# Kernel tuning notes

Measured on AMD Instinct MI355X. Metric: run time of the kernel, lower is better.

Reference implementation:

```python
import jax, jax.numpy as jnp
import numpy as np

B, L, E, H = 2, 2048, 2048, 16
HD = E // H  # 128
ROPE_BASE = 10000.0


def setup_inputs() -> dict:
    key = jax.random.key(0)
    k1, k2, k3 = jax.random.split(key, 3)
    x = jax.random.normal(k1, (B, L, E), dtype=jnp.float32)
    position_ids = jnp.tile(jnp.arange(L, dtype=jnp.int32)[None, :], (B, 1))
    # Linear weights stored as [in, out] so y = x @ W + b (equals torch x @ W.T + b)
    W_attn = jax.random.normal(k2, (E, 3 * E), dtype=jnp.float32) * (1.0 / np.sqrt(E))
    b_attn = jnp.zeros((3 * E,), dtype=jnp.float32)
    W_proj = jax.random.normal(k3, (E, E), dtype=jnp.float32) * (1.0 / np.sqrt(E))
    b_proj = jnp.zeros((E,), dtype=jnp.float32)
    return {"x": x, "position_ids": position_ids, "W_attn": W_attn,
            "b_attn": b_attn, "W_proj": W_proj, "b_proj": b_proj}


def _rotate_half(t):
    h = t.shape[-1] // 2
    return jnp.concatenate([-t[..., h:], t[..., :h]], axis=-1)


def _apply_rope(q, k, position_ids):
    # q,k: [B,H,L,HD]; position_ids: [B,L]
    inv_freq = 1.0 / (ROPE_BASE ** (jnp.arange(0, HD, 2, dtype=jnp.float32) / HD))
    angles = position_ids.astype(jnp.float32)[:, :, None] * inv_freq  # [B,L,HD/2]
    cos = jnp.concatenate([jnp.cos(angles)] * 2, axis=-1)[:, None]  # [B,1,L,HD]
    sin = jnp.concatenate([jnp.sin(angles)] * 2, axis=-1)[:, None]
    return q * cos + _rotate_half(q) * sin, k * cos + _rotate_half(k) * sin


def reference(x, position_ids, W_attn, b_attn, W_proj, b_proj):
    # fused QKV projection
    qkv = x @ W_attn + b_attn                       # [B,L,3E]
    q, k, v = jnp.split(qkv, 3, axis=-1)            # each [B,L,E]
    reshape = lambda t: t.reshape(B, L, H, HD).transpose(0, 2, 1, 3)  # [B,H,L,HD]
    q, k, v = reshape(q), reshape(k), reshape(v)
    q, k = _apply_rope(q, k, position_ids)
    # scaled dot-product attention (mask=None -> full attention, dropout 0)
    scores = jnp.einsum('bhqd,bhkd->bhqk', q, k) * (1.0 / np.sqrt(HD))
    probs = jax.nn.softmax(scores, axis=-1)
    y = jnp.einsum('bhqk,bhkd->bhqd', probs, v)     # [B,H,L,HD]
    y = y.transpose(0, 2, 1, 3).reshape(B, L, E)
    return y @ W_proj + b_proj
```

## Files before the change

### kernel.cpp

```cpp
#include <hip/hip_runtime.h>
#include <math.h>

#define BB 2
#define LL 2048
#define EE 2048
#define HH 16
#define HD 128
#define N3E (3*EE)

typedef __attribute__((ext_vector_type(8))) short  bf16x8;
typedef __attribute__((ext_vector_type(4))) float  f32x4;

__device__ __forceinline__ ushort f2bf(float f) {
    union { float f; unsigned u; } v; v.f = f;
    unsigned u = v.u + 0x7FFFu + ((v.u >> 16) & 1u);
    return (ushort)(u >> 16);
}
__device__ __forceinline__ float bf2f(ushort u) {
    union { unsigned u; float f; } v; v.u = ((unsigned)u) << 16;
    return v.f;
}

__global__ __launch_bounds__(256) void cvt_bf16(const float* __restrict__ in,
                                                ushort* __restrict__ out, int n) {
    int i = (blockIdx.x * 256 + threadIdx.x) * 8;
    float4 a = *(const float4*)(in + i);
    float4 b = *(const float4*)(in + i + 4);
    ushort4 p0 = { f2bf(a.x), f2bf(a.y), f2bf(a.z), f2bf(a.w) };
    ushort4 p1 = { f2bf(b.x), f2bf(b.y), f2bf(b.z), f2bf(b.w) };
    *(ushort4*)(out + i)     = p0;
    *(ushort4*)(out + i + 4) = p1;
}

__global__ __launch_bounds__(256) void transpose_bf16(const float* __restrict__ in,
                                                      ushort* __restrict__ out,
                                                      int R, int Ccol) {
    __shared__ float tile[32][33];
    int c0 = blockIdx.x * 32, r0 = blockIdx.y * 32;
    int t = threadIdx.x;
    int lr = t >> 5, lc = t & 31;
    #pragma unroll
    for (int i = 0; i < 4; ++i)
        tile[lr + i * 8][lc] = in[(size_t)(r0 + lr + i * 8) * Ccol + c0 + lc];
    __syncthreads();
    #pragma unroll
    for (int i = 0; i < 4; ++i)
        out[(size_t)(c0 + lr + i * 8) * R + r0 + lc] = f2bf(tile[lc][lr + i * 8]);
}

template<int WRITE_BF16>
__global__ __launch_bounds__(256) void gemm_bt_bf16(const ushort* __restrict__ A,
                                                    const ushort* __restrict__ Bt,
                                                    const float* __restrict__ bias,
                                                    void* __restrict__ C,
                                                    int M, int N, int K) {
    __shared__ __align__(16) ushort As[128 * 32];
    __shared__ __align__(16) ushort Bs[128 * 32];
    const int t    = threadIdx.x;
    const int lane = t & 63, w = t >> 6;
    const int m    = lane & 15, quad = lane >> 4;
    const int wm   = w >> 1, wn = w & 1;
    const int m0   = blockIdx.y * 128, n0 = blockIdx.x * 128;

    f32x4 acc[4][4];
    #pragma unroll
    for (int i = 0; i < 4; ++i)
        #pragma unroll
        for (int j = 0; j < 4; ++j) acc[i][j] = (f32x4){0.f, 0.f, 0.f, 0.f};

    for (int k0 = 0; k0 < K; k0 += 32) {
        __syncthreads();
        #pragma unroll
        for (int i = 0; i < 2; ++i) {
            int c = t + i * 256;
            int row = c >> 2, kc = c & 3;
            __builtin_amdgcn_global_load_lds(
                (const __attribute__((address_space(1))) unsigned int*)(A + (size_t)(m0 + row) * K + k0 + kc * 8),
                (__attribute__((address_space(3))) unsigned int*)(As + c * 8),
                16, 0, 0);
        }
        #pragma unroll
        for (int i = 0; i < 2; ++i) {
            int c = t + i * 256;
            int row = c >> 2, kc = c & 3;
            __builtin_amdgcn_global_load_lds(
                (const __attribute__((address_space(1))) unsigned int*)(Bt + (size_t)(n0 + row) * K + k0 + kc * 8),
                (__attribute__((address_space(3))) unsigned int*)(Bs + c * 8),
                16, 0, 0);
        }
        __syncthreads();
        bf16x8 af[4], bfr[4];
        #pragma unroll
        for (int mt = 0; mt < 4; ++mt)
            af[mt] = *(const bf16x8*)&As[(wm * 64 + mt * 16 + m) * 32 + quad * 8];
        #pragma unroll
        for (int nt = 0; nt < 4; ++nt)
            bfr[nt] = *(const bf16x8*)&Bs[(wn * 64 + nt * 16 + m) * 32 + quad * 8];
        #pragma unroll
        for (int mt = 0; mt < 4; ++mt)
            #pragma unroll
            for (int nt = 0; nt < 4; ++nt)
                acc[mt][nt] = __builtin_amdgcn_mfma_f32_16x16x32_bf16(af[mt], bfr[nt], acc[mt][nt], 0, 0, 0);
    }
    #pragma unroll
    for (int mt = 0; mt < 4; ++mt) {
        #pragma unroll
        for (int nt = 0; nt < 4; ++nt) {
            #pragma unroll
            for (int r = 0; r < 4; ++r) {
                int row = m0 + wm * 64 + mt * 16 + quad * 4 + r;
                int col = n0 + wn * 64 + nt * 16 + m;
                float v = acc[mt][nt][r] + bias[col];
                if (WRITE_BF16) ((ushort*)C)[(size_t)row * N + col] = f2bf(v);
                else            ((float*)C)[(size_t)row * N + col] = v;
            }
        }
    }
}

__global__ __launch_bounds__(256) void prep_qk(const ushort* __restrict__ qkvb,
                                               const int* __restrict__ pos_ids,
                                               ushort* __restrict__ Qt,
                                               ushort* __restrict__ Kt) {
    const float scale = 0.08838834764831845f;
    const float nl2b = -0.20762050593046014f;
    int idx = blockIdx.x * 256 + threadIdx.x;
    int p    = idx & 15;
    int r    = (idx >> 4) & 63;
    int tile = (idx >> 10) & 31;
    int h    = (idx >> 15) & 15;
    int b    = idx >> 19;
    int c    = p ^ (r & 15);
    int l    = tile * 64 + r;
    int half = c >> 3, cl = c & 7;
    const ushort* row = qkvb + (size_t)(b * LL + l) * N3E;
    float pos = (float)pos_ids[b * LL + l];

    bf16x8 qa = *(const bf16x8*)(row + h * HD + c * 8);
    bf16x8 qb = *(const bf16x8*)(row + h * HD + (c ^ 8) * 8);
    bf16x8 ka = *(const bf16x8*)(row + EE + h * HD + c * 8);
    bf16x8 kb = *(const bf16x8*)(row + EE + h * HD + (c ^ 8) * 8);
    bf16x8 qo, ko;
    #pragma unroll
    for (int i = 0; i < 8; ++i) {
        int j = cl * 8 + i;
        float ang = pos * exp2f((float)j * nl2b);
        float s, cs;
        sincosf(ang, &s, &cs);
        float sgn = half ? s : -s;
        float q1 = bf2f((ushort)qa[i]), q2 = bf2f((ushort)qb[i]);
        float k1 = bf2f((ushort)ka[i]), k2 = bf2f((ushort)kb[i]);
        qo[i] = (short)f2bf((q1 * cs + q2 * sgn) * scale);
        ko[i] = (short)f2bf(k1 * cs + k2 * sgn);
    }
    size_t obase = ((size_t)(b * 16 + h) * 32 + tile) * 8192 + r * 128 + p * 8;
    *(bf16x8*)(Qt + obase) = qo;
    *(bf16x8*)(Kt + obase) = ko;
}

__global__ __launch_bounds__(256) void prep_v(const ushort* __restrict__ qkvb,
                                              ushort* __restrict__ Vtt) {
    int idx = blockIdx.x * 256 + threadIdx.x;
    int p    = idx & 7;
    int r    = (idx >> 3) & 127;
    int tile = (idx >> 10) & 31;
    int h    = (idx >> 15) & 15;
    int b    = idx >> 19;
    int c    = p ^ (r & 7);
    int col  = 2 * EE + h * HD + r;
    bf16x8 o;
    #pragma unroll
    for (int i = 0; i < 8; ++i) {
        int kk = tile * 64 + c * 8 + i;
        o[i] = (short)qkvb[(size_t)(b * LL + kk) * N3E + col];
    }
    *(bf16x8*)(Vtt + ((size_t)(b * 16 + h) * 32 + tile) * 8192 + r * 64 + p * 8) = o;
}

#define PSTR 68

__global__ __launch_bounds__(256, 2) void flash2(const ushort* __restrict__ Qt,
                                                 const ushort* __restrict__ Kt,
                                                 const ushort* __restrict__ Vtt,
                                                 ushort* __restrict__ y) {
    __shared__ __align__(16) ushort Ks[64 * 128];
    __shared__ __align__(16) ushort Vs[128 * 64];
    __shared__ __align__(16) ushort Ps[4 * 32 * PSTR];

    const int t    = threadIdx.x;
    const int w    = t >> 6;
    const int lane = t & 63;
    const int m    = lane & 15;
    const int quad = lane >> 4;
    const int qblk = blockIdx.x;
    const int bh   = blockIdx.y;
    const int b    = bh >> 4, h = bh & 15;

    const ushort* Qhead = Qt  + (size_t)bh * 32 * 8192;
    const ushort* Khead = Kt  + (size_t)bh * 32 * 8192;
    const ushort* Vhead = Vtt + (size_t)bh * 32 * 8192;

    bf16x8 qf[2][4];
    #pragma unroll
    for (int mt = 0; mt < 2; ++mt) {
        int rloc = w * 32 + mt * 16 + m;
        const ushort* qtile = Qhead + (size_t)(qblk * 2 + (rloc >> 6)) * 8192
                              + (rloc & 63) * 128;
        #pragma unroll
        for (int ks = 0; ks < 4; ++ks)
            qf[mt][ks] = *(const bf16x8*)(qtile + ((ks * 4 + quad) ^ m) * 8);
    }

    f32x4 oacc[2][8];
    #pragma unroll
    for (int mt = 0; mt < 2; ++mt)
        #pragma unroll
        for (int dt = 0; dt < 8; ++dt) oacc[mt][dt] = (f32x4){0.f, 0.f, 0.f, 0.f};
    float m_i[8], l_pl[8];
    #pragma unroll
    for (int s = 0; s < 8; ++s) { m_i[s] = -INFINITY; l_pl[s] = 0.f; }

    {
        const ushort* ksrc = Khead;
        #pragma unroll
        for (int i = 0; i < 4; ++i) {
            int cid = t + i * 256;
            __builtin_amdgcn_global_load_lds(
                (const __attribute__((address_space(1))) unsigned int*)(ksrc + cid * 8),
                (__attribute__((address_space(3))) unsigned int*)(Ks + cid * 8),
                16, 0, 0);
        }
    }

    for (int kt = 0; kt < 32; ++kt) {
        asm volatile("s_waitcnt vmcnt(0)\n\ts_barrier" ::: "memory");

        {
            const ushort* vsrc = Vhead + (size_t)kt * 8192;
            #pragma unroll
            for (int i = 0; i < 4; ++i) {
                int cid = t + i * 256;
                __builtin_amdgcn_global_load_lds(
                    (const __attribute__((address_space(1))) unsigned int*)(vsrc + cid * 8),
                    (__attribute__((address_space(3))) unsigned int*)(Vs + cid * 8),
                    16, 0, 0);
            }
        }

        f32x4 sacc[2][4];
        #pragma unroll
        for (int mt = 0; mt < 2; ++mt)
            #pragma unroll
            for (int nt = 0; nt < 4; ++nt) sacc[mt][nt] = (f32x4){0.f, 0.f, 0.f, 0.f};
        __builtin_amdgcn_s_setprio(1);
        #pragma unroll
        for (int ks = 0; ks < 4; ++ks) {
            #pragma unroll
            for (int nt = 0; nt < 4; ++nt) {
                bf16x8 kf = *(const bf16x8*)&Ks[(nt * 16 + m) * 128 + (((ks * 4 + quad) ^ m)) * 8];
                sacc[0][nt] = __builtin_amdgcn_mfma_f32_16x16x32_bf16(qf[0][ks], kf, sacc[0][nt], 0, 0, 0);
                sacc[1][nt] = __builtin_amdgcn_mfma_f32_16x16x32_bf16(qf[1][ks], kf, sacc[1][nt], 0, 0, 0);
            }
        }
        __builtin_amdgcn_s_setprio(0);

        float alpha_s[2][4];
        #pragma unroll
        for (int mt = 0; mt < 2; ++mt) {
            #pragma unroll
            for (int r = 0; r < 4; ++r) {
                int slot = mt * 4 + r;
                float mx = fmaxf(fmaxf(sacc[mt][0][r], sacc[mt][1][r]),
                                 fmaxf(sacc[mt][2][r], sacc[mt][3][r]));
                #pragma unroll
                for (int off = 1; off < 16; off <<= 1) mx = fmaxf(mx, __shfl_xor(mx, off, 64));
                float mnew = fmaxf(m_i[slot], mx);
                float al = __expf(m_i[slot] - mnew);
                m_i[slot] = mnew;
                float rs = 0.f;
                #pragma unroll
                for (int nt = 0; nt < 4; ++nt) {
                    float pv = __expf(sacc[mt][nt][r] - mnew);
                    sacc[mt][nt][r] = pv;
                    rs += pv;
                }
                l_pl[slot] = l_pl[slot] * al + rs;
                alpha_s[mt][r] = al;
            }
        }
        #pragma unroll
        for (int mt = 0; mt < 2; ++mt)
            #pragma unroll
            for (int dt = 0; dt < 8; ++dt)
                #pragma unroll
                for (int r = 0; r < 4; ++r) oacc[mt][dt][r] *= alpha_s[mt][r];

        #pragma unroll
        for (int mt = 0; mt < 2; ++mt)
            #pragma unroll
            for (int nt = 0; nt < 4; ++nt)
                #pragma unroll
                for (int r = 0; r < 4; ++r)
                    Ps[w * 32 * PSTR + (mt * 16 + quad * 4 + r) * PSTR + nt * 16 + m]
                        = f2bf(sacc[mt][nt][r]);

        asm volatile("s_waitcnt vmcnt(0)\n\ts_barrier" ::: "memory");

        if (kt + 1 < 32) {
            const ushort* ksrc = Khead + (size_t)(kt + 1) * 8192;
            #pragma unroll
            for (int i = 0; i < 4; ++i) {
                int cid = t + i * 256;
                __builtin_amdgcn_global_load_lds(
                    (const __attribute__((address_space(1))) unsigned int*)(ksrc + cid * 8),
                    (__attribute__((address_space(3))) unsigned int*)(Ks + cid * 8),
                    16, 0, 0);
            }
        }

        __builtin_amdgcn_s_setprio(1);
        #pragma unroll
        for (int ks2 = 0; ks2 < 2; ++ks2) {
            bf16x8 pf0 = *(const bf16x8*)&Ps[w * 32 * PSTR + (0 * 16 + m) * PSTR + ks2 * 32 + quad * 8];
            bf16x8 pf1 = *(const bf16x8*)&Ps[w * 32 * PSTR + (1 * 16 + m) * PSTR + ks2 * 32 + quad * 8];
            #pragma unroll
            for (int dt = 0; dt < 8; ++dt) {
                bf16x8 vf = *(const bf16x8*)&Vs[(dt * 16 + m) * 64 + (((ks2 * 4 + quad) ^ (m & 7))) * 8];
                oacc[0][dt] = __builtin_amdgcn_mfma_f32_16x16x32_bf16(pf0, vf, oacc[0][dt], 0, 0, 0);
                oacc[1][dt] = __builtin_amdgcn_mfma_f32_16x16x32_bf16(pf1, vf, oacc[1][dt], 0, 0, 0);
            }
        }
        __builtin_amdgcn_s_setprio(0);
    }

    #pragma unroll
    for (int s = 0; s < 8; ++s) {
        #pragma unroll
        for (int off = 1; off < 16; off <<= 1) l_pl[s] += __shfl_xor(l_pl[s], off, 64);
        l_pl[s] = 1.0f / l_pl[s];
    }
    #pragma unroll
    for (int mt = 0; mt < 2; ++mt) {
        #pragma unroll
        for (int dt = 0; dt < 8; ++dt) {
            #pragma unroll
            for (int r = 0; r < 4; ++r) {
                int row = qblk * 128 + w * 32 + mt * 16 + quad * 4 + r;
                y[(size_t)(b * LL + row) * EE + h * HD + dt * 16 + m]
                    = f2bf(oacc[mt][dt][r] * l_pl[mt * 4 + r]);
            }
        }
    }
}

extern "C" void kernel_launch(void* const* d_in, const int* in_sizes, int n_in,
                              void* d_out, int out_size, void* d_ws, size_t ws_size,
                              hipStream_t stream) {
    const float* x      = (const float*)d_in[0];
    const int*   pos    = (const int*)d_in[1];
    const float* W_attn = (const float*)d_in[2];
    const float* b_attn = (const float*)d_in[3];
    const float* W_proj = (const float*)d_in[4];
    const float* b_proj = (const float*)d_in[5];
    float* out = (float*)d_out;

    const int M = BB * LL;
    ushort* xb   = (ushort*)d_ws;
    ushort* Wat  = xb   + (size_t)M * EE;
    ushort* Wpt  = Wat  + (size_t)N3E * EE;
    ushort* qkvb = Wpt  + (size_t)EE * EE;
    ushort* Kt   = qkvb + (size_t)M * N3E;
    ushort* Vtt  = Kt   + (size_t)M * EE;
    ushort* Qt   = xb;
    ushort* yb   = Wat;

    dim3 blk(256);
    cvt_bf16<<<dim3(M * EE / (256 * 8)), blk, 0, stream>>>(x, xb, M * EE);
    transpose_bf16<<<dim3(N3E / 32, EE / 32), blk, 0, stream>>>(W_attn, Wat, EE, N3E);
    transpose_bf16<<<dim3(EE / 32, EE / 32), blk, 0, stream>>>(W_proj, Wpt, EE, EE);

    gemm_bt_bf16<1><<<dim3(N3E / 128, M / 128), blk, 0, stream>>>(
        xb, Wat, b_attn, qkvb, M, N3E, EE);

    prep_qk<<<dim3(4096), blk, 0, stream>>>(qkvb, pos, Qt, Kt);
    prep_v<<<dim3(4096), blk, 0, stream>>>(qkvb, Vtt);

    flash2<<<dim3(LL / 128, BB * HH), blk, 0, stream>>>(Qt, Kt, Vtt, yb);

    gemm_bt_bf16<0><<<dim3(EE / 128, M / 128), blk, 0, stream>>>(
        yb, Wpt, b_proj, out, M, EE, EE);
}
```

Measured before the change: 473.9 us.

## Replace QKV GEMM with 256x256-tile, 4-stage async-LDS pipelined kernel

Adds a new GEMM kernel for the QKV projection. It uses 256x256 output tiles with 512 threads and a 4-slot LDS ring filled by direct global-to-LDS loads, split into two phases per k-step with barriers and priority bumps around the MFMA blocks. It also swizzles the block index so neighbouring workgroups map to XCD-friendly tiles, and uses an XOR-swizzled LDS layout to avoid bank conflicts. The aim is higher MFMA utilization and more operand reuse than the old 128x128 kernel. In exchange it needs more registers and LDS (64KB), which limits occupancy, and relies on careful vmcnt accounting.

After: 467.4 us. No clear change (-1.4%).

```diff
diff --git a/kernel.cpp b/kernel.cpp
--- a/kernel.cpp
+++ b/kernel.cpp
@@ -46,6 +46,130 @@
     #pragma unroll
     for (int i = 0; i < 4; ++i)
         out[(size_t)(c0 + lr + i * 8) * R + r0 + lc] = f2bf(tile[lc][lr + i * 8]);
+}
+
+template<int WRITE_BF16>
+__global__ __launch_bounds__(512, 2) void gemm256_8ph(const ushort* __restrict__ A,
+                                                      const ushort* __restrict__ Bt,
+                                                      const float* __restrict__ bias,
+                                                      void* __restrict__ C,
+                                                      int M, int N, int K, int nby) {
+    __shared__ __align__(16) ushort Asl[4 * 8192];
+    __shared__ __align__(16) ushort Bsl[4 * 8192];
+
+    const int t    = threadIdx.x;
+    const int lane = t & 63;
+    const int w    = t >> 6;
+    const int m    = lane & 15;
+    const int quad = lane >> 4;
+    const int wm   = w >> 2;
+    const int wn   = w & 3;
+
+    const int nwg = gridDim.x;
+    const int cpx = nwg >> 3;
+    const int swz = ((int)blockIdx.x & 7) * cpx + ((int)blockIdx.x >> 3);
+    const int by  = swz % nby;
+    const int bx  = swz / nby;
+    const int m0  = by * 256, n0 = bx * 256;
+
+    const int r16s  = (t >> 2) & 15;
+    const int kels  = ((t & 3) ^ ((t & 32) ? 2 : 0)) * 8;
+    const int row0s = ((t >> 6) << 4) + r16s;
+    const int row1s = row0s + 128;
+
+    const int foff = m * 32 + ((quad * 8) ^ ((m & 8) ? 16 : 0));
+
+#define STAGE_A(T_) do { int _s = (T_) & 3; \
+    __builtin_amdgcn_global_load_lds( \
+        (const __attribute__((address_space(1))) unsigned int*)(A + (size_t)(m0 + row0s) * K + (T_) * 32 + kels), \
+        (__attribute__((address_space(3))) unsigned int*)(Asl + _s * 8192 + t * 8), 16, 0, 0); \
+    __builtin_amdgcn_global_load_lds( \
+        (const __attribute__((address_space(1))) unsigned int*)(A + (size_t)(m0 + row1s) * K + (T_) * 32 + kels), \
+        (__attribute__((address_space(3))) unsigned int*)(Asl + _s * 8192 + (512 + t) * 8), 16, 0, 0); } while (0)
+#define STAGE_B(T_) do { int _s = (T_) & 3; \
+    __builtin_amdgcn_global_load_lds( \
+        (const __attribute__((address_space(1))) unsigned int*)(Bt + (size_t)(n0 + row0s) * K + (T_) * 32 + kels), \
+        (__attribute__((address_space(3))) unsigned int*)(Bsl + _s * 8192 + t * 8), 16, 0, 0); \
+    __builtin_amdgcn_global_load_lds( \
+        (const __attribute__((address_space(1))) unsigned int*)(Bt + (size_t)(n0 + row1s) * K + (T_) * 32 + kels), \
+        (__attribute__((address_space(3))) unsigned int*)(Bsl + _s * 8192 + (512 + t) * 8), 16, 0, 0); } while (0)
+
+    f32x4 acc[8][4];
+    #pragma unroll
+    for (int i = 0; i < 8; ++i)
+        #pragma unroll
+        for (int j = 0; j < 4; ++j) acc[i][j] = (f32x4){0.f, 0.f, 0.f, 0.f};
+
+    const int NT = K >> 5;
+
+    STAGE_A(0); STAGE_B(0);
+    STAGE_A(1); STAGE_B(1);
+    STAGE_A(2); STAGE_B(2);
+    asm volatile("s_waitcnt vmcnt(8)" ::: "memory");
+    __builtin_amdgcn_s_barrier();
+
+    for (int T = 0; T < NT; ++T) {
+        const int slot = T & 3;
+        const ushort* as = Asl + slot * 8192 + wm * 4096;
+        const ushort* bs = Bsl + slot * 8192 + wn * 2048;
+
+        bf16x8 af[4], bf[4];
+        #pragma unroll
+        for (int mt = 0; mt < 4; ++mt)
+            af[mt] = *(const bf16x8*)(as + mt * 512 + foff);
+        #pragma unroll
+        for (int nt = 0; nt < 4; ++nt)
+            bf[nt] = *(const bf16x8*)(bs + nt * 512 + foff);
+        if (T + 3 < NT) STAGE_A(T + 3);
+        __builtin_amdgcn_s_barrier();
+        asm volatile("s_waitcnt lgkmcnt(0)" ::: "memory");
+        __builtin_amdgcn_s_setprio(1);
+        #pragma unroll
+        for (int mt = 0; mt < 4; ++mt)
+            #pragma unroll
+            for (int nt = 0; nt < 4; ++nt)
+                acc[mt][nt] = __builtin_amdgcn_mfma_f32_16x16x32_bf16(af[mt], bf[nt], acc[mt][nt], 0, 0, 0);
+        __builtin_amdgcn_s_setprio(0);
+        __builtin_amdgcn_s_barrier();
+
+        #pragma unroll
+        for (int mt = 0; mt < 4; ++mt)
+            af[mt] = *(const bf16x8*)(as + (4 + mt) * 512 + foff);
+        if (T + 3 < NT) STAGE_B(T + 3);
+        if (T + 3 < NT)      asm volatile("s_waitcnt vmcnt(8)" ::: "memory");
+        else if (T + 2 < NT) asm volatile("s_waitcnt vmcnt(4)" ::: "memory");
+        else                 asm volatile("s_waitcnt vmcnt(0)" ::: "memory");
+        __builtin_amdgcn_s_barrier();
+        asm volatile("s_waitcnt lgkmcnt(0)" ::: "memory");
+        __builtin_amdgcn_s_setprio(1);
+        #pragma unroll
+        for (int mt = 0; mt < 4; ++mt)
+            #pragma unroll
+            for (int nt = 0; nt < 4; ++nt)
+                acc[4 + mt][nt] = __builtin_amdgcn_mfma_f32_16x16x32_bf16(af[mt], bf[nt], acc[4 + mt][nt], 0, 0, 0);
+        __builtin_amdgcn_s_setprio(0);
+        __builtin_amdgcn_s_barrier();
+    }
+#undef STAGE_A
+#undef STAGE_B
+
+    float bcol[4];
+    #pragma unroll
+    for (int nt = 0; nt < 4; ++nt) bcol[nt] = bias[n0 + wn * 64 + nt * 16 + m];
+    #pragma unroll
+    for (int mt = 0; mt < 8; ++mt) {
+        #pragma unroll
+        for (int nt = 0; nt < 4; ++nt) {
+            #pragma unroll
+            for (int r = 0; r < 4; ++r) {
+                int row = m0 + wm * 128 + mt * 16 + quad * 4 + r;
+                int col = n0 + wn * 64 + nt * 16 + m;
+                float v = acc[mt][nt][r] + bcol[nt];
+                if (WRITE_BF16) ((ushort*)C)[(size_t)row * N + col] = f2bf(v);
+                else            ((float*)C)[(size_t)row * N + col] = v;
+            }
+        }
+    }
 }
 
 template<int WRITE_BF16>
@@ -379,8 +503,8 @@
     transpose_bf16<<<dim3(N3E / 32, EE / 32), blk, 0, stream>>>(W_attn, Wat, EE, N3E);
     transpose_bf16<<<dim3(EE / 32, EE / 32), blk, 0, stream>>>(W_proj, Wpt, EE, EE);
 
-    gemm_bt_bf16<1><<<dim3(N3E / 128, M / 128), blk, 0, stream>>>(
-        xb, Wat, b_attn, qkvb, M, N3E, EE);
+    gemm256_8ph<1><<<dim3((M / 256) * (N3E / 256)), dim3(512), 0, stream>>>(
+        xb, Wat, b_attn, qkvb, M, N3E, EE, M / 256);
 
     prep_qk<<<dim3(4096), blk, 0, stream>>>(qkvb, pos, Qt, Kt);
     prep_v<<<dim3(4096), blk, 0, stream>>>(qkvb, Vtt);
```

## Rewrite GEMMs with 4-stage LDS pipeline, 256x128 tiles, swizzled LDS and block order

Applied to the files above, without the earlier changes.

Replaces the single-buffered 128x128 GEMM with a 512-thread, 256x128 tile kernel that keeps three K-tiles of async global-to-LDS loads in flight in a 4-slot ring buffer, using explicit vmcnt waits and barriers. It adds an XOR swizzle on the LDS layout to reduce bank conflicts, remaps blocks into an XCD-aware order for L2 locality, raises wave priority around the MFMA block, and hoists bias loads. The aim is to hide global memory latency behind MFMA work in both projection GEMMs. In exchange it uses more LDS per block and relies on hand-written waitcnt bookkeeping, so miscounting outstanding loads could race.

New measurement: 458.1 us. 3.3% less time.

```diff
diff --git a/kernel.cpp b/kernel.cpp
--- a/kernel.cpp
+++ b/kernel.cpp
@@ -49,18 +49,46 @@
 }
 
 template<int WRITE_BF16>
-__global__ __launch_bounds__(256) void gemm_bt_bf16(const ushort* __restrict__ A,
-                                                    const ushort* __restrict__ Bt,
-                                                    const float* __restrict__ bias,
-                                                    void* __restrict__ C,
-                                                    int M, int N, int K) {
-    __shared__ __align__(16) ushort As[128 * 32];
-    __shared__ __align__(16) ushort Bs[128 * 32];
+__global__ __launch_bounds__(512, 2) void gemm_ktile(const ushort* __restrict__ A,
+                                                     const ushort* __restrict__ Bt,
+                                                     const float* __restrict__ bias,
+                                                     void* __restrict__ C,
+                                                     int M, int N, int K, int nby) {
+    __shared__ __align__(16) ushort Asl[4 * 8192];
+    __shared__ __align__(16) ushort Bsl[4 * 4096];
+
     const int t    = threadIdx.x;
-    const int lane = t & 63, w = t >> 6;
-    const int m    = lane & 15, quad = lane >> 4;
-    const int wm   = w >> 1, wn = w & 1;
-    const int m0   = blockIdx.y * 128, n0 = blockIdx.x * 128;
+    const int lane = t & 63;
+    const int w    = t >> 6;
+    const int m    = lane & 15;
+    const int quad = lane >> 4;
+    const int wm   = w >> 1;
+    const int wn   = w & 1;
+
+    const int nwg = gridDim.x;
+    const int cpx = nwg >> 3;
+    const int swz = ((int)blockIdx.x & 7) * cpx + ((int)blockIdx.x >> 3);
+    const int by  = swz % nby;
+    const int bx  = swz / nby;
+    const int m0  = by * 256, n0 = bx * 128;
+
+    const int r16s  = (t >> 2) & 15;
+    const int kels  = ((t & 3) ^ ((t & 32) ? 2 : 0)) * 8;
+    const int row0s = ((t >> 6) << 4) + r16s;
+    const int row1s = row0s + 128;
+
+    const int foff = m * 32 + ((quad * 8) ^ ((m & 8) ? 16 : 0));
+
+#define STAGE(T_) do { int _s = (T_) & 3; \
+    __builtin_amdgcn_global_load_lds( \
+        (const __attribute__((address_space(1))) unsigned int*)(A + (size_t)(m0 + row0s) * K + (T_) * 32 + kels), \
+        (__attribute__((address_space(3))) unsigned int*)(Asl + _s * 8192 + t * 8), 16, 0, 0); \
+    __builtin_amdgcn_global_load_lds( \
+        (const __attribute__((address_space(1))) unsigned int*)(A + (size_t)(m0 + row1s) * K + (T_) * 32 + kels), \
+        (__attribute__((address_space(3))) unsigned int*)(Asl + _s * 8192 + (512 + t) * 8), 16, 0, 0); \
+    __builtin_amdgcn_global_load_lds( \
+        (const __attribute__((address_space(1))) unsigned int*)(Bt + (size_t)(n0 + row0s) * K + (T_) * 32 + kels), \
+        (__attribute__((address_space(3))) unsigned int*)(Bsl + _s * 4096 + t * 8), 16, 0, 0); } while (0)
 
     f32x4 acc[4][4];
     #pragma unroll
@@ -68,40 +96,46 @@
         #pragma unroll
         for (int j = 0; j < 4; ++j) acc[i][j] = (f32x4){0.f, 0.f, 0.f, 0.f};
 
-    for (int k0 = 0; k0 < K; k0 += 32) {
-        __syncthreads();
-        #pragma unroll
-        for (int i = 0; i < 2; ++i) {
-            int c = t + i * 256;
-            int row = c >> 2, kc = c & 3;
-            __builtin_amdgcn_global_load_lds(
-                (const __attribute__((address_space(1))) unsigned int*)(A + (size_t)(m0 + row) * K + k0 + kc * 8),
-                (__attribute__((address_space(3))) unsigned int*)(As + c * 8),
-                16, 0, 0);
-        }
-        #pragma unroll
-        for (int i = 0; i < 2; ++i) {
-            int c = t + i * 256;
-            int row = c >> 2, kc = c & 3;
-            __builtin_amdgcn_global_load_lds(
-                (const __attribute__((address_space(1))) unsigned int*)(Bt + (size_t)(n0 + row) * K + k0 + kc * 8),
-                (__attribute__((address_space(3))) unsigned int*)(Bs + c * 8),
-                16, 0, 0);
-        }
-        __syncthreads();
-        bf16x8 af[4], bfr[4];
+    const int NT = K >> 5;
+
+    STAGE(0); STAGE(1); STAGE(2);
+    asm volatile("s_waitcnt vmcnt(6)" ::: "memory");
+    __builtin_amdgcn_s_barrier();
+
+    for (int T = 0; T < NT; ++T) {
+        const int slot = T & 3;
+        const ushort* as = Asl + slot * 8192 + wm * 2048;
+        const ushort* bs = Bsl + slot * 4096 + wn * 2048;
+
+        bf16x8 af[4], bf[4];
         #pragma unroll
         for (int mt = 0; mt < 4; ++mt)
-            af[mt] = *(const bf16x8*)&As[(wm * 64 + mt * 16 + m) * 32 + quad * 8];
+            af[mt] = *(const bf16x8*)(as + mt * 512 + foff);
         #pragma unroll
         for (int nt = 0; nt < 4; ++nt)
-            bfr[nt] = *(const bf16x8*)&Bs[(wn * 64 + nt * 16 + m) * 32 + quad * 8];
+            bf[nt] = *(const bf16x8*)(bs + nt * 512 + foff);
+
+        if (T + 3 < NT) STAGE(T + 3);
+
+        if (T + 3 < NT)      asm volatile("s_waitcnt vmcnt(6)" ::: "memory");
+        else if (T + 2 < NT) asm volatile("s_waitcnt vmcnt(3)" ::: "memory");
+        else                 asm volatile("s_waitcnt vmcnt(0)" ::: "memory");
+        __builtin_amdgcn_s_barrier();
+        asm volatile("s_waitcnt lgkmcnt(0)" ::: "memory");
+        __builtin_amdgcn_s_setprio(1);
         #pragma unroll
         for (int mt = 0; mt < 4; ++mt)
             #pragma unroll
             for (int nt = 0; nt < 4; ++nt)
-                acc[mt][nt] = __builtin_amdgcn_mfma_f32_16x16x32_bf16(af[mt], bfr[nt], acc[mt][nt], 0, 0, 0);
-    }
+                acc[mt][nt] = __builtin_amdgcn_mfma_f32_16x16x32_bf16(af[mt], bf[nt], acc[mt][nt], 0, 0, 0);
+        __builtin_amdgcn_s_setprio(0);
+        __builtin_amdgcn_s_barrier();
+    }
+#undef STAGE
+
+    float bcol[4];
+    #pragma unroll
+    for (int nt = 0; nt < 4; ++nt) bcol[nt] = bias[n0 + wn * 64 + nt * 16 + m];
     #pragma unroll
     for (int mt = 0; mt < 4; ++mt) {
         #pragma unroll
@@ -110,7 +144,7 @@
             for (int r = 0; r < 4; ++r) {
                 int row = m0 + wm * 64 + mt * 16 + quad * 4 + r;
                 int col = n0 + wn * 64 + nt * 16 + m;
-                float v = acc[mt][nt][r] + bias[col];
+                float v = acc[mt][nt][r] + bcol[nt];
                 if (WRITE_BF16) ((ushort*)C)[(size_t)row * N + col] = f2bf(v);
                 else            ((float*)C)[(size_t)row * N + col] = v;
             }
@@ -379,14 +413,14 @@
     transpose_bf16<<<dim3(N3E / 32, EE / 32), blk, 0, stream>>>(W_attn, Wat, EE, N3E);
     transpose_bf16<<<dim3(EE / 32, EE / 32), blk, 0, stream>>>(W_proj, Wpt, EE, EE);
 
-    gemm_bt_bf16<1><<<dim3(N3E / 128, M / 128), blk, 0, stream>>>(
-        xb, Wat, b_attn, qkvb, M, N3E, EE);
+    gemm_ktile<1><<<dim3((M / 256) * (N3E / 128)), dim3(512), 0, stream>>>(
+        xb, Wat, b_attn, qkvb, M, N3E, EE, M / 256);
 
     prep_qk<<<dim3(4096), blk, 0, stream>>>(qkvb, pos, Qt, Kt);
     prep_v<<<dim3(4096), blk, 0, stream>>>(qkvb, Vtt);
 
     flash2<<<dim3(LL / 128, BB * HH), blk, 0, stream>>>(Qt, Kt, Vtt, yb);
 
-    gemm_bt_bf16<0><<<dim3(EE / 128, M / 128), blk, 0, stream>>>(
-        yb, Wpt, b_proj, out, M, EE, EE);
-}
+    gemm_ktile<0><<<dim3((M / 256) * (EE / 128)), dim3(512), 0, stream>>>(
+        yb, Wpt, b_proj, out, M, EE, EE, M / 256);
+}
```
